# Kernel tuning notes

Hardware: AMD Instinct MI355X
Metric: run time of the kernel (lower is better)

The kernel has to match this reference:

```python
import jax, jax.numpy as jnp
import numpy as np

H = 5  # hidden size (hardcoded in the torch module)


def setup_inputs() -> dict:
    key = jax.random.key(0)
    ks = jax.random.split(key, 9)
    N, T = 32768, 600
    s = 1.0 / np.sqrt(H)  # torch LSTM/Linear init scale (uniform bound), use as stddev
    return {
        "x": jax.random.normal(ks[0], (N, T), dtype=jnp.float32),
        "w_ih": jax.random.normal(ks[1], (4 * H, 1), dtype=jnp.float32) * s,
        "w_hh": jax.random.normal(ks[2], (4 * H, H), dtype=jnp.float32) * s,
        "b_ih": jax.random.normal(ks[3], (4 * H,), dtype=jnp.float32) * s,
        "b_hh": jax.random.normal(ks[4], (4 * H,), dtype=jnp.float32) * s,
        "fc_w": jax.random.normal(ks[5], (15, H), dtype=jnp.float32) * s,
        "fc_b": jax.random.normal(ks[6], (15,), dtype=jnp.float32) * s,
        "out_w": jax.random.normal(ks[7], (1, 15), dtype=jnp.float32) * (1.0 / np.sqrt(15)),
        "out_b": jax.random.normal(ks[8], (1,), dtype=jnp.float32) * (1.0 / np.sqrt(15)),
    }


def reference(x, w_ih, w_hh, b_ih, b_hh, fc_w, fc_b, out_w, out_b):
    # x: (N, T) -> unsqueeze to feature dim of 1 is implicit (input_size=1).
    N = x.shape[0]
    b = b_ih + b_hh  # (4H,)
    w_ih_vec = w_ih[:, 0]  # (4H,) since input_size == 1

    def step(carry, x_t):
        h, c = carry  # (N, H) each
        # gates: (N, 4H); PyTorch gate order: i, f, g, o
        gates = x_t[:, None] * w_ih_vec + h @ w_hh.T + b
        i = jax.nn.sigmoid(gates[:, 0 * H:1 * H])
        f = jax.nn.sigmoid(gates[:, 1 * H:2 * H])
        g = jnp.tanh(gates[:, 2 * H:3 * H])
        o = jax.nn.sigmoid(gates[:, 3 * H:4 * H])
        c = f * c + i * g
        h = o * jnp.tanh(c)
        return (h, c), None

    h0 = jnp.zeros((N, H), dtype=x.dtype)
    c0 = jnp.zeros((N, H), dtype=x.dtype)
    (h_T, _), _ = jax.lax.scan(step, (h0, c0), x.T)  # scan over time: xs (T, N)
    # Head: only the last timestep's hidden state is used.
    hid = h_T @ fc_w.T + fc_b          # (N, 15)
    out = hid @ out_w.T + out_b        # (N, 1)
    return jax.nn.sigmoid(out)
```

## Files before the change

### kernel.cpp

```cpp
#include <hip/hip_runtime.h>
#include <math.h>


#define LOG2E 1.44269504088896340736f

typedef float v2f __attribute__((ext_vector_type(2)));

constexpr int T_ = 600;
constexpr int SEQ_PER_BLOCK = 32;
constexpr int TTILE = 64;
constexpr int LDS_STRIDE = 68;

__device__ __forceinline__ float fast_rcp(float v)  { return __builtin_amdgcn_rcpf(v); }
__device__ __forceinline__ float fast_exp2(float v) { return __builtin_amdgcn_exp2f(v); }

template <int CTRL>
__device__ __forceinline__ float dpp_q(float v) {
    const int x = __float_as_int(v);
    return __int_as_float(__builtin_amdgcn_update_dpp(x, x, CTRL, 0xF, 0xF, false));
}

__global__ __launch_bounds__(64, 1) void lstm_kernel(
    const float* __restrict__ x,
    const float* __restrict__ w_ih,
    const float* __restrict__ w_hh,
    const float* __restrict__ b_ih,
    const float* __restrict__ b_hh,
    const float* __restrict__ fc_w,
    const float* __restrict__ fc_b,
    const float* __restrict__ out_w,
    const float* __restrict__ out_b,
    float* __restrict__ out)
{
    __shared__ float xs[SEQ_PER_BLOCK * LDS_STRIDE];

    const int lane = threadIdx.x;
    const int s    = lane >> 1;
    const int half = lane & 1;
    const int seq  = blockIdx.x * SEQ_PER_BLOCK + s;

    const int rloT[2][5] = {{0, 1, 2, 5, 6}, {3, 4, 7, 8, 9}};
    const int rhiT[2][5] = {{10, 11, 12, 15, 16}, {13, 14, 17, 18, 19}};
    const int gtT [2][5] = {{1, 1, 1, 0, 0}, {1, 1, 0, 0, 0}};

    v2f wih2[5], bb2[5], whh2[5][5];
#pragma unroll
    for (int p = 0; p < 5; ++p) {
        const int rlo = rloT[half][p], rhi = rhiT[half][p];
        const float sl = -LOG2E;
        const float sh = gtT[half][p] ? (-2.0f * LOG2E) : (-LOG2E);
        wih2[p] = (v2f){ w_ih[rlo] * sl, w_ih[rhi] * sh };
        bb2[p]  = (v2f){ (b_ih[rlo] + b_hh[rlo]) * sl,
                         (b_ih[rhi] + b_hh[rhi]) * sh };
#pragma unroll
        for (int k = 0; k < 5; ++k)
            whh2[p][k] = (v2f){ w_hh[rlo * 5 + k] * sl, w_hh[rhi * 5 + k] * sh };
    }
    const int ng = half ? 2 : 3;

    float H[5] = {0.f, 0.f, 0.f, 0.f, 0.f};
    float cA = 0.f, cB = 0.f, cC = 0.f;

    const float* xblk = x + (size_t)(blockIdx.x * SEQ_PER_BLOCK) * T_;

    auto step = [&](float xt) {
        const v2f x2 = (v2f){ xt, xt };
        v2f g2[5];
#pragma unroll
        for (int p = 0; p < 5; ++p) g2[p] = x2 * wih2[p] + bb2[p];
#pragma unroll
        for (int k = 0; k < 5; ++k) {
            const v2f h2 = (v2f){ H[k], H[k] };
#pragma unroll
            for (int p = 0; p < 5; ++p) g2[p] += h2 * whh2[p][k];
        }
        v2f act2[5];
#pragma unroll
        for (int p = 0; p < 5; ++p) {
            const float dx = 1.0f + fast_exp2(g2[p].x);
            const float dy = 1.0f + fast_exp2(g2[p].y);
            const float rp = fast_rcp(dx * dy);
            act2[p].x = rp * dy;
            act2[p].y = rp * dx;
        }
#pragma unroll
        for (int p = 0; p < 3; ++p)
            if (p < ng)
                act2[p].y = fmaf(act2[p].y, -4.0f * LOG2E, 2.0f * LOG2E);
        const float PA = act2[0].x * act2[0].y;
        const float PB = act2[1].x * act2[1].y;
        const float P2 = dpp_q<0xA0>(act2[2].x * act2[2].y);
        const float f2 = dpp_q<0xF5>(act2[2].x);
        const float o2 = dpp_q<0xF5>(act2[2].y);
        cA = fmaf(act2[3].x, cA, PA);
        cB = fmaf(act2[4].x, cB, PB);
        cC = fmaf(f2, cC, P2);
        const float dA = 1.0f + fast_exp2(cA);
        const float dB = 1.0f + fast_exp2(cB);
        const float dC = 1.0f + fast_exp2(cC);
        const float q  = fast_rcp(dA * dB);
        const float tA = fmaf(q * dB, 2.0f, -1.0f);
        const float tB = fmaf(q * dA, 2.0f, -1.0f);
        const float tC = fmaf(fast_rcp(dC), 2.0f, -1.0f);
        const float hA = act2[3].y * tA;
        const float hB = act2[4].y * tB;
        H[0] = dpp_q<0xA0>(hA);
        H[1] = dpp_q<0xA0>(hB);
        H[2] = o2 * tC;
        H[3] = dpp_q<0xF5>(hA);
        H[4] = dpp_q<0xF5>(hB);
    };

    const int rrow = lane >> 4;
    const int ccol = (lane & 15) << 2;

    for (int t0i = 0; t0i < T_; t0i += TTILE) {
        __syncthreads();
#pragma unroll
        for (int it = 0; it < 8; ++it) {
            const int r = it * 4 + rrow;
            if (t0i + ccol < T_) {
                const float4 v = *(const float4*)(xblk + (size_t)r * T_ + (t0i + ccol));
                *(float4*)&xs[r * LDS_STRIDE + ccol] = v;
            }
        }
        __syncthreads();

        const int steps = min(TTILE, T_ - t0i);
        const float* xr = &xs[s * LDS_STRIDE];
        for (int tt = 0; tt < steps; tt += 4) {
            const float4 xv4 = *(const float4*)&xr[tt];
            step(xv4.x);
            step(xv4.y);
            step(xv4.z);
            step(xv4.w);
        }
    }

    if (half == 0) {
        float acc = out_b[0];
#pragma unroll
        for (int j = 0; j < 15; ++j) {
            float hid = fc_b[j];
#pragma unroll
            for (int k = 0; k < 5; ++k) hid = fmaf(H[k], fc_w[j * 5 + k], hid);
            acc = fmaf(hid, out_w[j], acc);
        }
        out[seq] = fast_rcp(1.0f + fast_exp2(-acc * LOG2E));
    }
}

extern "C" void kernel_launch(void* const* d_in, const int* in_sizes, int n_in,
                              void* d_out, int out_size, void* d_ws, size_t ws_size,
                              hipStream_t stream) {
    const float* x    = (const float*)d_in[0];
    const float* w_ih = (const float*)d_in[1];
    const float* w_hh = (const float*)d_in[2];
    const float* b_ih = (const float*)d_in[3];
    const float* b_hh = (const float*)d_in[4];
    const float* fc_w = (const float*)d_in[5];
    const float* fc_b = (const float*)d_in[6];
    const float* out_w = (const float*)d_in[7];
    const float* out_b = (const float*)d_in[8];
    float* out = (float*)d_out;

    const int N = in_sizes[0] / T_;
    const int grid = N / SEQ_PER_BLOCK;
    hipLaunchKernelGGL(lstm_kernel, dim3(grid), dim3(64), 0, stream,
                       x, w_ih, w_hh, b_ih, b_hh, fc_w, fc_b, out_w, out_b, out);
}
```

Measured before the change: 258.3 us.

## Double-buffer x tiles in LDS with register prefetch of next tile

Loads for the next time tile are issued into registers before the current tile's recurrence runs, then written into the other half of a double-buffered LDS array afterward. This hides global-load latency behind the serial LSTM steps and drops one barrier per tile. It also software-pipelines the per-thread float4 LDS reads one group ahead. It costs 32 extra VGPRs for the prefetch buffer and doubles LDS. The last tile's prefetch is clamped to stay in bounds, which makes it a redundant load.

```diff
diff --git a/kernel.cpp b/kernel.cpp
--- a/kernel.cpp
+++ b/kernel.cpp
@@ -9,7 +9,9 @@
 constexpr int T_ = 600;
 constexpr int SEQ_PER_BLOCK = 32;
 constexpr int TTILE = 64;
+constexpr int NTILES = (T_ + TTILE - 1) / TTILE;
 constexpr int LDS_STRIDE = 68;
+constexpr int XBUF = SEQ_PER_BLOCK * LDS_STRIDE;
 
 __device__ __forceinline__ float fast_rcp(float v)  { return __builtin_amdgcn_rcpf(v); }
 __device__ __forceinline__ float fast_exp2(float v) { return __builtin_amdgcn_exp2f(v); }
@@ -32,7 +34,7 @@
     const float* __restrict__ out_b,
     float* __restrict__ out)
 {
-    __shared__ float xs[SEQ_PER_BLOCK * LDS_STRIDE];
+    __shared__ float xs[2 * XBUF];
 
     const int lane = threadIdx.x;
     const int s    = lane >> 1;
@@ -114,27 +116,42 @@
     const int rrow = lane >> 4;
     const int ccol = (lane & 15) << 2;
 
-    for (int t0i = 0; t0i < T_; t0i += TTILE) {
-        __syncthreads();
+#pragma unroll
+    for (int it = 0; it < 8; ++it) {
+        const int r = it * 4 + rrow;
+        const float4 v = *(const float4*)(xblk + (size_t)r * T_ + ccol);
+        *(float4*)&xs[r * LDS_STRIDE + ccol] = v;
+    }
+    __syncthreads();
+
+    for (int tile = 0; tile < NTILES; ++tile) {
+        const int tpf  = (tile + 1 < NTILES) ? (tile + 1) : (NTILES - 1);
+        const int cpf  = (tpf * TTILE + ccol <= T_ - 4) ? (tpf * TTILE + ccol) : (T_ - 4);
+        float4 pf[8];
 #pragma unroll
         for (int it = 0; it < 8; ++it) {
             const int r = it * 4 + rrow;
-            if (t0i + ccol < T_) {
-                const float4 v = *(const float4*)(xblk + (size_t)r * T_ + (t0i + ccol));
-                *(float4*)&xs[r * LDS_STRIDE + ccol] = v;
-            }
+            pf[it] = *(const float4*)(xblk + (size_t)r * T_ + cpf);
+        }
+        const int t0i   = tile * TTILE;
+        const int steps = (T_ - t0i >= TTILE) ? TTILE : (T_ - t0i);
+        const float* xr = &xs[(tile & 1) * XBUF + s * LDS_STRIDE];
+        float4 cur = *(const float4*)&xr[0];
+        for (int tt = 0; tt < steps; tt += 4) {
+            const float4 nxt = *(const float4*)&xr[tt + 4];
+            step(cur.x);
+            step(cur.y);
+            step(cur.z);
+            step(cur.w);
+            cur = nxt;
+        }
+        float* xw = &xs[((tile + 1) & 1) * XBUF];
+#pragma unroll
+        for (int it = 0; it < 8; ++it) {
+            const int r = it * 4 + rrow;
+            *(float4*)&xw[r * LDS_STRIDE + ccol] = pf[it];
         }
         __syncthreads();
-
-        const int steps = min(TTILE, T_ - t0i);
-        const float* xr = &xs[s * LDS_STRIDE];
-        for (int tt = 0; tt < steps; tt += 4) {
-            const float4 xv4 = *(const float4*)&xr[tt];
-            step(xv4.x);
-            step(xv4.y);
-            step(xv4.z);
-            step(xv4.w);
-        }
     }
 
     if (half == 0) {
```

After: 248.0 us. 1.04x faster.
